# Performance work log

Measured on AMD Instinct MI355X. Metric: run time of the kernel, lower is better.

## Reference

```python
import jax, jax.numpy as jnp
import numpy as np

HEADS = 16
DIM_HEAD = 64
SCALE = DIM_HEAD ** -0.5


def setup_inputs() -> dict:
    key = jax.random.key(0)
    k1, k2, k3, k4 = jax.random.split(key, 4)
    dim = 1024
    inner = HEADS * DIM_HEAD  # 1024
    b, n = 4, 2048
    x = jax.random.normal(k1, (b, n, dim), dtype=jnp.float32)
    # weights stored as [in, out] (equivalent math to torch Linear)
    w_qkv = jax.random.normal(k2, (dim, inner * 3), dtype=jnp.float32) * (dim ** -0.5)
    w_out = jax.random.normal(k3, (inner, dim), dtype=jnp.float32) * (inner ** -0.5)
    b_out = jax.random.normal(k4, (dim,), dtype=jnp.float32) * 0.01
    return {"x": x, "w_qkv": w_qkv, "w_out": w_out, "b_out": b_out}


def reference(x, w_qkv, w_out, b_out):
    b, n, dim = x.shape
    qkv = x @ w_qkv                                   # [b, n, 3*inner]
    q, k, v = jnp.split(qkv, 3, axis=-1)
    def to_heads(t):
        return t.reshape(b, n, HEADS, DIM_HEAD).transpose(0, 2, 1, 3)  # b h n d
    q, k, v = to_heads(q) * SCALE, to_heads(k), to_heads(v)
    dots = jnp.einsum('bhid,bhjd->bhij', q, k)        # [b, h, n, n]
    mask_value = -jnp.finfo(dots.dtype).max
    causal_mask = jnp.triu(jnp.ones((n, n), dtype=bool), k=1)
    dots = jnp.where(causal_mask, mask_value, dots)
    attn = jax.nn.softmax(dots, axis=-1)
    out = jnp.einsum('bhij,bhjd->bhid', attn, v)      # [b, h, n, d]
    out = out.transpose(0, 2, 1, 3).reshape(b, n, HEADS * DIM_HEAD)
    return out @ w_out + b_out
```

## Files before the change

### kernel.cpp

```cpp
#include <hip/hip_runtime.h>
#include <hip/hip_bf16.h>
#include <stdint.h>

typedef __attribute__((ext_vector_type(8))) short bf16x8;
typedef __attribute__((ext_vector_type(4))) float f32x4;
typedef __attribute__((ext_vector_type(4))) unsigned int uint32x4;

#define TOKENS 8192
#define DMODEL 1024
#define NQKV   3072
#define NSEQ   2048
#define NHEAD  16
#define DHEAD  64

__device__ __forceinline__ ushort f32_bf16(float f) {
    uint32_t u = __builtin_bit_cast(uint32_t, f);
    u = (u + 0x7fffu + ((u >> 16) & 1u)) >> 16;
    return (ushort)u;
}

__device__ __forceinline__ unsigned int cvt_pk_bf16(float lo, float hi) {
    unsigned int r;
    asm("v_cvt_pk_bf16_f32 %0, %1, %2" : "=v"(r) : "v"(lo), "v"(hi));
    return r;
}
__device__ __forceinline__ void permlane32_swap(unsigned int& a, unsigned int& b) {
    asm("v_permlane32_swap_b32 %0, %1" : "+v"(a), "+v"(b));
}
__device__ __forceinline__ void permlane16_swap(unsigned int& a, unsigned int& b) {
    asm("v_permlane16_swap_b32 %0, %1" : "+v"(a), "+v"(b));
}
__device__ __forceinline__ unsigned opaque_copy(unsigned x) {
    unsigned y;
    asm("v_mov_b32 %0, %1" : "=v"(y) : "v"(x));
    return y;
}

__device__ __forceinline__ float red_max_g(float x) {
    unsigned a = __builtin_bit_cast(unsigned, x);
    unsigned b = opaque_copy(a);
    permlane16_swap(a, b);
    float r = fmaxf(__builtin_bit_cast(float, a), __builtin_bit_cast(float, b));
    unsigned c = __builtin_bit_cast(unsigned, r);
    unsigned d = opaque_copy(c);
    permlane32_swap(c, d);
    return fmaxf(__builtin_bit_cast(float, c), __builtin_bit_cast(float, d));
}
__device__ __forceinline__ float red_sum_g(float x) {
    unsigned a = __builtin_bit_cast(unsigned, x);
    unsigned b = opaque_copy(a);
    permlane16_swap(a, b);
    float r = __builtin_bit_cast(float, a) + __builtin_bit_cast(float, b);
    unsigned c = __builtin_bit_cast(unsigned, r);
    unsigned d = opaque_copy(c);
    permlane32_swap(c, d);
    return __builtin_bit_cast(float, c) + __builtin_bit_cast(float, d);
}

__device__ __forceinline__ void gload16(const void* g, void* l) {
    __builtin_amdgcn_global_load_lds(
        (const __attribute__((address_space(1))) void*)g,
        (__attribute__((address_space(3))) void*)l, 16, 0, 0);
}

__device__ __forceinline__ void barf() {
    asm volatile("" ::: "memory");
    __builtin_amdgcn_s_barrier();
    asm volatile("" ::: "memory");
}

__global__ void cvt_x_kernel(const float* __restrict__ x, ushort* __restrict__ xb) {
    int i = blockIdx.x * 256 + threadIdx.x;
    float4 v = reinterpret_cast<const float4*>(x)[i];
    ushort4 o;
    o.x = f32_bf16(v.x); o.y = f32_bf16(v.y);
    o.z = f32_bf16(v.z); o.w = f32_bf16(v.w);
    reinterpret_cast<ushort4*>(xb)[i] = o;
}

__global__ __launch_bounds__(256) void cvt_wt_kernel(
    const float* __restrict__ w, ushort* __restrict__ wt, int N)
{
    __shared__ float tile[64][65];
    const int tid = threadIdx.x;
    const int r  = tid >> 4;
    const int c4 = (tid & 15) * 4;
    const int n0 = blockIdx.x * 64;
    const int k0 = blockIdx.y * 64;
    #pragma unroll
    for (int i = 0; i < 4; ++i) {
        const float4 v = *reinterpret_cast<const float4*>(&w[(size_t)(k0 + r + i * 16) * N + n0 + c4]);
        tile[r + i * 16][c4 + 0] = v.x;
        tile[r + i * 16][c4 + 1] = v.y;
        tile[r + i * 16][c4 + 2] = v.z;
        tile[r + i * 16][c4 + 3] = v.w;
    }
    __syncthreads();
    #pragma unroll
    for (int i = 0; i < 4; ++i) {
        ushort4 o;
        o.x = f32_bf16(tile[c4 + 0][r + i * 16]);
        o.y = f32_bf16(tile[c4 + 1][r + i * 16]);
        o.z = f32_bf16(tile[c4 + 2][r + i * 16]);
        o.w = f32_bf16(tile[c4 + 3][r + i * 16]);
        *reinterpret_cast<ushort4*>(&wt[(size_t)(n0 + r + i * 16) * 1024 + k0 + c4]) = o;
    }
}

template<int MODE>
__global__ __launch_bounds__(256) void gemm_bt(
    const ushort* __restrict__ A, const ushort* __restrict__ Bt,
    ushort* __restrict__ Qb, ushort* __restrict__ Kb, ushort* __restrict__ Vtb,
    float* __restrict__ Out, const float* __restrict__ bias)
{
    constexpr int K = 1024;
    __shared__ __align__(16) ushort As[2][128 * 32];
    __shared__ __align__(16) ushort Bs[2][128 * 32];

    const int lane = threadIdx.x & 63;
    const int w    = threadIdx.x >> 6;
    const int l16  = lane & 15;
    const int g    = lane >> 4;
    const int row0 = blockIdx.y * 128;
    const int col0 = blockIdx.x * 128;
    const int wr   = (w >> 1) * 64;
    const int wc   = (w & 1) * 64;

    const int srow  = w * 16 + (lane >> 2);
    const int sswz8 = ((lane & 3) ^ ((lane >> 3) & 3)) * 8;
    const ushort* Ag = A  + (size_t)(row0 + srow) * K + sswz8;
    const ushort* Bg = Bt + (size_t)(col0 + srow) * K + sswz8;
    const int woff = w * (16 * 32);

    const int cq8 = (g ^ ((l16 >> 1) & 3)) * 8;

    f32x4 acc[4][4] = {};

#define GSTAGE(BUF, KK) do {                                             \
        gload16(Ag + (KK),          &As[BUF][woff]);                     \
        gload16(Ag + 64 * K + (KK), &As[BUF][woff + 64 * 32]);           \
        gload16(Bg + (KK),          &Bs[BUF][woff]);                     \
        gload16(Bg + 64 * K + (KK), &Bs[BUF][woff + 64 * 32]);           \
    } while (0)

#define GCOMPUTE(BUF) do {                                               \
        bf16x8 a[4], b[4];                                               \
        _Pragma("unroll")                                                \
        for (int m = 0; m < 4; ++m)                                      \
            a[m] = *reinterpret_cast<const bf16x8*>(                     \
                &As[BUF][(wr + m * 16 + l16) * 32 + cq8]);               \
        _Pragma("unroll")                                                \
        for (int n = 0; n < 4; ++n)                                      \
            b[n] = *reinterpret_cast<const bf16x8*>(                     \
                &Bs[BUF][(wc + n * 16 + l16) * 32 + cq8]);               \
        _Pragma("unroll")                                                \
        for (int m = 0; m < 4; ++m)                                      \
            _Pragma("unroll")                                            \
            for (int n = 0; n < 4; ++n)                                  \
                acc[m][n] = __builtin_amdgcn_mfma_f32_16x16x32_bf16(     \
                    a[m], b[n], acc[m][n], 0, 0, 0);                     \
    } while (0)

    GSTAGE(0, 0);
    GSTAGE(1, 32);
    for (int kk = 0; kk + 128 <= K; kk += 64) {
        asm volatile("s_waitcnt vmcnt(4)" ::: "memory");
        barf();
        GCOMPUTE(0);
        barf();
        GSTAGE(0, kk + 64);
        asm volatile("s_waitcnt vmcnt(4)" ::: "memory");
        barf();
        GCOMPUTE(1);
        barf();
        GSTAGE(1, kk + 96);
    }
    asm volatile("s_waitcnt vmcnt(4)" ::: "memory");
    barf();
    GCOMPUTE(0);
    asm volatile("s_waitcnt vmcnt(0)" ::: "memory");
    barf();
    GCOMPUTE(1);
#undef GSTAGE
#undef GCOMPUTE

    if (MODE == 0) {
        const int part = col0 >> 10;
        const float QSC = 0.18033688011112042f;
        #pragma unroll
        for (int m = 0; m < 4; ++m) {
            const int trow = row0 + wr + m * 16 + 4 * g;
            #pragma unroll
            for (int n = 0; n < 4; ++n) {
                const int c  = col0 + wc + n * 16 + l16;
                const int cc = c & 1023;
                const int h  = cc >> 6, d = cc & 63;
                #pragma unroll
                for (int jj = 0; jj < 4; ++jj) {
                    const int t  = trow + jj;
                    const int bb = t >> 11, nn = t & 2047;
                    const float v = acc[m][n][jj];
                    const size_t bhid = (size_t)(bb * NHEAD + h);
                    if (part == 0)
                        Qb[(bhid * NSEQ + nn) * DHEAD + d] = f32_bf16(v * QSC);
                    else if (part == 1)
                        Kb[(bhid * NSEQ + nn) * DHEAD + d] = f32_bf16(v);
                    else
                        Vtb[bhid * (NSEQ * DHEAD) + (size_t)(nn >> 5) * (DHEAD * 32)
                            + d * 32 + (nn & 31)] = f32_bf16(v);
                }
            }
        }
    } else {
        #pragma unroll
        for (int m = 0; m < 4; ++m) {
            const int trow = row0 + wr + m * 16 + 4 * g;
            #pragma unroll
            for (int n = 0; n < 4; ++n) {
                const int c = col0 + wc + n * 16 + l16;
                const float bv = bias[c];
                #pragma unroll
                for (int jj = 0; jj < 4; ++jj)
                    Out[(size_t)(trow + jj) * DMODEL + c] = acc[m][n][jj] + bv;
            }
        }
    }
}

__device__ __forceinline__ void attn_qk(
    int kt, int qr0s, int l16, int g,
    const bf16x8 (&kk)[4][2],
    const bf16x8 qf0, const bf16x8 qf1,
    f32x4 (&oacc)[4], float& mrun, float& lsum,
    bf16x8& pf0, bf16x8& pf1)
{
    const f32x4 zero = {};
    f32x4 s[4];
    __builtin_amdgcn_s_setprio(1);
    #pragma unroll
    for (int t = 0; t < 4; ++t) {
        s[t] = __builtin_amdgcn_mfma_f32_16x16x32_bf16(kk[t][0], qf0, zero, 0, 0, 0);
        s[t] = __builtin_amdgcn_mfma_f32_16x16x32_bf16(kk[t][1], qf1, s[t], 0, 0, 0);
    }
    __builtin_amdgcn_s_setprio(0);
    if (kt + 63 > qr0s) {
        const int kb = kt + 4 * g - (qr0s + l16);
        #pragma unroll
        for (int t = 0; t < 4; ++t)
            #pragma unroll
            for (int jj = 0; jj < 4; ++jj)
                if (kb + 16 * t + jj > 0) s[t][jj] = -1e30f;
    }
    const float m0 = fmaxf(fmaxf(s[0][0], s[0][1]), s[0][2]);
    const float m1 = fmaxf(fmaxf(s[0][3], s[1][0]), s[1][1]);
    const float m2 = fmaxf(fmaxf(s[1][2], s[1][3]), s[2][0]);
    const float m3 = fmaxf(fmaxf(s[2][1], s[2][2]), s[2][3]);
    const float m4 = fmaxf(fmaxf(s[3][0], s[3][1]), s[3][2]);
    const float m5 = fmaxf(fmaxf(m0, m1), m2);
    const float m6 = fmaxf(fmaxf(m3, m4), s[3][3]);
    const float mxl = fmaxf(m5, m6);
    if (__any(mxl > mrun + 8.0f)) {
        const float mx = red_max_g(mxl);
        const float mn = fmaxf(mrun, mx);
        const float sc = __builtin_amdgcn_exp2f(mrun - mn);
        mrun = mn;
        lsum *= sc;
        float scj[4];
        #pragma unroll
        for (int jj = 0; jj < 4; ++jj) scj[jj] = __shfl(sc, 4 * g + jj);
        #pragma unroll
        for (int dt = 0; dt < 4; ++dt)
            #pragma unroll
            for (int jj = 0; jj < 4; ++jj) oacc[dt][jj] *= scj[jj];
    }
    float ps = 0.f;
    unsigned int pw[4][2];
    #pragma unroll
    for (int t = 0; t < 4; ++t) {
        const float p0 = __builtin_amdgcn_exp2f(s[t][0] - mrun);
        const float p1 = __builtin_amdgcn_exp2f(s[t][1] - mrun);
        const float p2 = __builtin_amdgcn_exp2f(s[t][2] - mrun);
        const float p3 = __builtin_amdgcn_exp2f(s[t][3] - mrun);
        ps += (p0 + p1) + (p2 + p3);
        pw[t][0] = cvt_pk_bf16(p0, p1);
        pw[t][1] = cvt_pk_bf16(p2, p3);
    }
    lsum += ps;
    unsigned int a0 = pw[0][0], a1 = pw[0][1], b0 = pw[1][0], b1 = pw[1][1];
    permlane32_swap(a0, b0); permlane32_swap(a1, b1);
    permlane16_swap(a0, b0); permlane16_swap(a1, b1);
    pf0 = __builtin_bit_cast(bf16x8, (uint32x4){a0, a1, b0, b1});
    unsigned int c0 = pw[2][0], c1 = pw[2][1], d0 = pw[3][0], d1 = pw[3][1];
    permlane32_swap(c0, d0); permlane32_swap(c1, d1);
    permlane16_swap(c0, d0); permlane16_swap(c1, d1);
    pf1 = __builtin_bit_cast(bf16x8, (uint32x4){c0, c1, d0, d1});
}

__global__ __launch_bounds__(256) void attn_kernel(
    const ushort* __restrict__ Qb, const ushort* __restrict__ Kb,
    const ushort* __restrict__ Vt, ushort* __restrict__ Ob)
{
    __shared__ __align__(16) ushort Klds[2][4096];
    __shared__ __align__(16) ushort Vlds[2][4096];

    const int lane = threadIdx.x & 63;
    const int w    = threadIdx.x >> 6;
    const int l16  = lane & 15;
    const int g    = lane >> 4;

    const int bid = blockIdx.x;
    const int xcd = bid & 7, ii = bid >> 3;
    const int bh  = xcd * 8 + (ii >> 4);
    const int jlo = ii & 15;
    const int jhi = 31 - jlo;

    const int qr0_lo = jlo * 64 + w * 16;
    const int qr0_hi = jhi * 64 + w * 16;
    const int nt = jhi + 1;

    const ushort* QpL = Qb + ((size_t)bh * NSEQ + qr0_lo + l16) * DHEAD + 8 * g;
    const ushort* QpH = Qb + ((size_t)bh * NSEQ + qr0_hi + l16) * DHEAD + 8 * g;
    const bf16x8 qfL0 = *reinterpret_cast<const bf16x8*>(QpL);
    const bf16x8 qfL1 = *reinterpret_cast<const bf16x8*>(QpL + 32);
    const bf16x8 qfH0 = *reinterpret_cast<const bf16x8*>(QpH);
    const bf16x8 qfH1 = *reinterpret_cast<const bf16x8*>(QpH + 32);

    const ushort* Kg = Kb + (size_t)bh * (NSEQ * DHEAD);
    const ushort* Vg = Vt + (size_t)bh * (NSEQ * DHEAD);

    const int q0    = w * 2;
    const int srow  = lane >> 2;
    const int sswz8 = ((lane & 3) ^ ((lane >> 3) & 3)) * 8;
    const int cq8   = (g ^ ((l16 >> 1) & 3)) * 8;

    f32x4 oaccL[4] = {}, oaccH[4] = {};
    float mrunL = -1e30f, lsumL = 0.f, mrunH = -1e30f, lsumH = 0.f;

    #pragma unroll
    for (int i = 0; i < 2; ++i) {
        const int q = q0 + i;
        gload16(Kg + (size_t)((q & 3) * 16 + srow) * 64 + (q >> 2) * 32 + sswz8,
                &Klds[0][q * 512]);
        gload16(Vg + (size_t)(q >> 2) * 2048 + ((q & 3) * 16 + srow) * 32 + sswz8,
                &Vlds[0][q * 512]);
    }
    __syncthreads();

    for (int t = 0; t < nt; ++t) {
        const int cur = t & 1;
        if (t + 1 < nt) {
            const int kt1 = (t + 1) * 64;
            #pragma unroll
            for (int i = 0; i < 2; ++i) {
                const int q = q0 + i;
                gload16(Kg + (size_t)(kt1 + (q & 3) * 16 + srow) * 64 + (q >> 2) * 32 + sswz8,
                        &Klds[cur ^ 1][q * 512]);
                gload16(Vg + (size_t)kt1 * 64 + (q >> 2) * 2048 + ((q & 3) * 16 + srow) * 32 + sswz8,
                        &Vlds[cur ^ 1][q * 512]);
            }
        }
        const int kt = t * 64;
        bf16x8 kk[4][2];
        #pragma unroll
        for (int tt = 0; tt < 4; ++tt) {
            #pragma unroll
            for (int h = 0; h < 2; ++h)
                kk[tt][h] = *reinterpret_cast<const bf16x8*>(
                    &Klds[cur][h * 2048 + (16 * tt + l16) * 32 + cq8]);
        }
        bf16x8 pfH0, pfH1, pfL0, pfL1;
        attn_qk(kt, qr0_hi, l16, g, kk, qfH0, qfH1, oaccH, mrunH, lsumH, pfH0, pfH1);
        const bool doLo = (t <= jlo);
        if (doLo)
            attn_qk(kt, qr0_lo, l16, g, kk, qfL0, qfL1, oaccL, mrunL, lsumL, pfL0, pfL1);
        __builtin_amdgcn_s_setprio(1);
        #pragma unroll
        for (int dt = 0; dt < 4; ++dt) {
            const bf16x8 v0 = *reinterpret_cast<const bf16x8*>(
                &Vlds[cur][(dt * 16 + l16) * 32 + cq8]);
            const bf16x8 v1 = *reinterpret_cast<const bf16x8*>(
                &Vlds[cur][2048 + (dt * 16 + l16) * 32 + cq8]);
            oaccH[dt] = __builtin_amdgcn_mfma_f32_16x16x32_bf16(pfH0, v0, oaccH[dt], 0, 0, 0);
            oaccH[dt] = __builtin_amdgcn_mfma_f32_16x16x32_bf16(pfH1, v1, oaccH[dt], 0, 0, 0);
            if (doLo) {
                oaccL[dt] = __builtin_amdgcn_mfma_f32_16x16x32_bf16(pfL0, v0, oaccL[dt], 0, 0, 0);
                oaccL[dt] = __builtin_amdgcn_mfma_f32_16x16x32_bf16(pfL1, v1, oaccL[dt], 0, 0, 0);
            }
        }
        __builtin_amdgcn_s_setprio(0);
        __syncthreads();
    }

    const int bb = bh >> 4, h = bh & 15;
    {
        const float inv = 1.0f / red_sum_g(lsumH);
        float invj[4];
        #pragma unroll
        for (int jj = 0; jj < 4; ++jj) invj[jj] = __shfl(inv, 4 * g + jj);
        #pragma unroll
        for (int jj = 0; jj < 4; ++jj) {
            const size_t t = (size_t)bb * NSEQ + qr0_hi + 4 * g + jj;
            #pragma unroll
            for (int dt = 0; dt < 4; ++dt)
                Ob[t * DMODEL + h * DHEAD + dt * 16 + l16] = f32_bf16(oaccH[dt][jj] * invj[jj]);
        }
    }
    {
        const float inv = 1.0f / red_sum_g(lsumL);
        float invj[4];
        #pragma unroll
        for (int jj = 0; jj < 4; ++jj) invj[jj] = __shfl(inv, 4 * g + jj);
        #pragma unroll
        for (int jj = 0; jj < 4; ++jj) {
            const size_t t = (size_t)bb * NSEQ + qr0_lo + 4 * g + jj;
            #pragma unroll
            for (int dt = 0; dt < 4; ++dt)
                Ob[t * DMODEL + h * DHEAD + dt * 16 + l16] = f32_bf16(oaccL[dt][jj] * invj[jj]);
        }
    }
}

extern "C" void kernel_launch(void* const* d_in, const int* in_sizes, int n_in,
                              void* d_out, int out_size, void* d_ws, size_t ws_size,
                              hipStream_t stream)
{
    const float* x     = (const float*)d_in[0];
    const float* w_qkv = (const float*)d_in[1];
    const float* w_out = (const float*)d_in[2];
    const float* b_out = (const float*)d_in[3];
    float* out = (float*)d_out;

    char* ws = (char*)d_ws;
    ushort* x_bf   = (ushort*)(ws);
    ushort* wqkv_t = (ushort*)(ws + 16777216);
    ushort* wout_t = (ushort*)(ws + 23068672);
    ushort* q_bf   = (ushort*)(ws + 25165824);
    ushort* k_bf   = (ushort*)(ws + 41943040);
    ushort* vt_bf  = (ushort*)(ws + 58720256);
    ushort* attn_bf = x_bf;

    cvt_x_kernel<<<dim3(TOKENS * DMODEL / 4 / 256), dim3(256), 0, stream>>>(x, x_bf);
    cvt_wt_kernel<<<dim3(NQKV / 64, 1024 / 64), dim3(256), 0, stream>>>(w_qkv, wqkv_t, NQKV);
    cvt_wt_kernel<<<dim3(1024 / 64, 1024 / 64), dim3(256), 0, stream>>>(w_out, wout_t, 1024);

    gemm_bt<0><<<dim3(NQKV / 128, TOKENS / 128), dim3(256), 0, stream>>>(
        x_bf, wqkv_t, q_bf, k_bf, vt_bf, nullptr, nullptr);

    attn_kernel<<<dim3(1024), dim3(256), 0, stream>>>(q_bf, k_bf, vt_bf, attn_bf);

    gemm_bt<1><<<dim3(DMODEL / 128, TOKENS / 128), dim3(256), 0, stream>>>(
        attn_bf, wout_t, nullptr, nullptr, nullptr, out, b_out);
}
```

Baseline: 208.9 us.

## Replace QKV GEMM with 256x256-tile, 512-thread kernel with swizzled block order

Adds a dedicated QKV projection GEMM that uses 256x256 output tiles, 8 waves per block, 64-wide K stages double-buffered in LDS with an XOR swizzle, and a phase-interleaved schedule that overlaps global loads with MFMA work. It also remaps block indices so that neighbouring blocks share input panels. The larger tile is meant to raise arithmetic intensity and cut redundant global and L2 traffic compared with the 128x128 template. The cost is more registers (128 accumulator floats per lane) and about 128KB of LDS per block, which limits occupancy to one block per CU. The output projection GEMM keeps the old kernel, now split out as its own non-template function.

```diff
diff --git a/kernel.cpp b/kernel.cpp
--- a/kernel.cpp
+++ b/kernel.cpp
@@ -107,10 +107,136 @@
     }
 }
 
-template<int MODE>
-__global__ __launch_bounds__(256) void gemm_bt(
+__global__ __launch_bounds__(512) void gemm256_qkv(
     const ushort* __restrict__ A, const ushort* __restrict__ Bt,
-    ushort* __restrict__ Qb, ushort* __restrict__ Kb, ushort* __restrict__ Vtb,
+    ushort* __restrict__ Qb, ushort* __restrict__ Kb, ushort* __restrict__ Vtb)
+{
+    constexpr int K = 1024;
+    __shared__ __align__(16) ushort Alds[2][2][128 * 64];
+    __shared__ __align__(16) ushort Blds[2][2][128 * 64];
+
+    const int tid  = threadIdx.x;
+    const int lane = tid & 63;
+    const int w    = tid >> 6;
+    const int l16  = lane & 15;
+    const int g    = lane >> 4;
+
+    const int gidx = (blockIdx.x & 7) * 48 + (blockIdx.x >> 3);
+    const int row0 = (gidx & 31) * 256;
+    const int col0 = (gidx >> 5) * 256;
+
+    const int wm   = w >> 2;
+    const int wn   = w & 3;
+    const int wrow = wm * 128;
+    const int wcol = wn * 64;
+
+    const int c0   = w * 2;
+    const int srow = lane >> 3;
+    const int sq   = ((lane & 7) ^ srow) * 8;
+    const ushort* Abase = A  + (size_t)(row0 + srow) * K + sq;
+    const ushort* Bbase = Bt + (size_t)(col0 + srow) * K + sq;
+
+    f32x4 acc[8][4] = {};
+    bf16x8 bfr[4][2];
+
+#define STAGE_A2(T) do { const size_t _k = (size_t)(T) * 64;                  \
+        gload16(Abase + _k + (size_t)(c0 * 8) * K,         &Alds[(T)&1][0][c0 * 512]);       \
+        gload16(Abase + _k + (size_t)((c0 + 1) * 8) * K,   &Alds[(T)&1][0][(c0 + 1) * 512]); \
+        gload16(Abase + _k + (size_t)(128 + c0 * 8) * K,   &Alds[(T)&1][1][c0 * 512]);       \
+        gload16(Abase + _k + (size_t)(128 + (c0 + 1) * 8) * K, &Alds[(T)&1][1][(c0 + 1) * 512]); \
+    } while (0)
+#define STAGE_B2(T) do { const size_t _k = (size_t)(T) * 64;                  \
+        gload16(Bbase + _k + (size_t)(c0 * 8) * K,         &Blds[(T)&1][0][c0 * 512]);       \
+        gload16(Bbase + _k + (size_t)((c0 + 1) * 8) * K,   &Blds[(T)&1][0][(c0 + 1) * 512]); \
+        gload16(Bbase + _k + (size_t)(128 + c0 * 8) * K,   &Blds[(T)&1][1][c0 * 512]);       \
+        gload16(Bbase + _k + (size_t)(128 + (c0 + 1) * 8) * K, &Blds[(T)&1][1][(c0 + 1) * 512]); \
+    } while (0)
+
+#define RD_A(D, M, KS) (*reinterpret_cast<const bf16x8*>(                     \
+    &Alds[D][wm][((M) * 16 + l16) * 64 + ((((KS) * 4 + g) ^ (l16 & 7)) * 8)]))
+#define RD_B(D, N, KS) (*reinterpret_cast<const bf16x8*>(                     \
+    &Blds[D][wn >> 1][((wn & 1) * 64 + (N) * 16 + l16) * 64 + ((((KS) * 4 + g) ^ (l16 & 7)) * 8)]))
+
+#define PHASE(D, MB, LOADB, STMT, VMSTMT) do {                                \
+        bf16x8 af00 = RD_A(D, MB, 0),     af01 = RD_A(D, MB, 1);              \
+        bf16x8 af10 = RD_A(D, (MB) + 1, 0), af11 = RD_A(D, (MB) + 1, 1);      \
+        if (LOADB) {                                                          \
+            _Pragma("unroll")                                                 \
+            for (int n = 0; n < 4; ++n) {                                     \
+                bfr[n][0] = RD_B(D, n, 0);                                    \
+                bfr[n][1] = RD_B(D, n, 1);                                    \
+            }                                                                 \
+        }                                                                     \
+        STMT;                                                                 \
+        barf();                                                               \
+        __builtin_amdgcn_s_setprio(1);                                        \
+        _Pragma("unroll")                                                     \
+        for (int n = 0; n < 4; ++n) {                                         \
+            acc[MB][n]       = __builtin_amdgcn_mfma_f32_16x16x32_bf16(af00, bfr[n][0], acc[MB][n], 0, 0, 0);       \
+            acc[MB][n]       = __builtin_amdgcn_mfma_f32_16x16x32_bf16(af01, bfr[n][1], acc[MB][n], 0, 0, 0);       \
+            acc[(MB) + 1][n] = __builtin_amdgcn_mfma_f32_16x16x32_bf16(af10, bfr[n][0], acc[(MB) + 1][n], 0, 0, 0); \
+            acc[(MB) + 1][n] = __builtin_amdgcn_mfma_f32_16x16x32_bf16(af11, bfr[n][1], acc[(MB) + 1][n], 0, 0, 0); \
+        }                                                                     \
+        __builtin_amdgcn_s_setprio(0);                                        \
+        VMSTMT;                                                               \
+        barf();                                                               \
+    } while (0)
+
+    STAGE_B2(0); STAGE_A2(0); STAGE_B2(1);
+    asm volatile("s_waitcnt vmcnt(4)" ::: "memory");
+    barf();
+
+    for (int i = 0; i < 8; ++i) {
+        const int ta = 2 * i, tb = 2 * i + 1;
+        const bool more = (i < 7);
+        PHASE(0, 0, true,  { STAGE_A2(tb); }, );
+        PHASE(0, 2, false, { if (more) STAGE_B2(ta + 2); }, );
+        PHASE(0, 4, false, , );
+        PHASE(0, 6, false, ,
+              { if (more) asm volatile("s_waitcnt vmcnt(4)" ::: "memory");
+                else      asm volatile("s_waitcnt vmcnt(0)" ::: "memory"); });
+        PHASE(1, 0, true,  { if (more) STAGE_A2(ta + 2); }, );
+        PHASE(1, 2, false, { if (more) STAGE_B2(tb + 2); }, );
+        PHASE(1, 4, false, , );
+        PHASE(1, 6, false, ,
+              { if (more) asm volatile("s_waitcnt vmcnt(4)" ::: "memory"); });
+    }
+#undef PHASE
+#undef RD_A
+#undef RD_B
+#undef STAGE_A2
+#undef STAGE_B2
+
+    const float QSC = 0.18033688011112042f;
+    const int part = col0 >> 10;
+    #pragma unroll
+    for (int m = 0; m < 8; ++m) {
+        const int trow = row0 + wrow + m * 16 + 4 * g;
+        #pragma unroll
+        for (int n = 0; n < 4; ++n) {
+            const int c  = col0 + wcol + n * 16 + l16;
+            const int cc = c & 1023;
+            const int h  = cc >> 6, d = cc & 63;
+            #pragma unroll
+            for (int jj = 0; jj < 4; ++jj) {
+                const int t  = trow + jj;
+                const int bb = t >> 11, nn = t & 2047;
+                const float v = acc[m][n][jj];
+                const size_t bhid = (size_t)(bb * NHEAD + h);
+                if (part == 0)
+                    Qb[(bhid * NSEQ + nn) * DHEAD + d] = f32_bf16(v * QSC);
+                else if (part == 1)
+                    Kb[(bhid * NSEQ + nn) * DHEAD + d] = f32_bf16(v);
+                else
+                    Vtb[bhid * (NSEQ * DHEAD) + (size_t)(nn >> 5) * (DHEAD * 32)
+                        + d * 32 + (nn & 31)] = f32_bf16(v);
+            }
+        }
+    }
+}
+
+__global__ __launch_bounds__(256) void gemm_out(
+    const ushort* __restrict__ A, const ushort* __restrict__ Bt,
     float* __restrict__ Out, const float* __restrict__ bias)
 {
     constexpr int K = 1024;
@@ -131,7 +257,6 @@
     const ushort* Ag = A  + (size_t)(row0 + srow) * K + sswz8;
     const ushort* Bg = Bt + (size_t)(col0 + srow) * K + sswz8;
     const int woff = w * (16 * 32);
-
     const int cq8 = (g ^ ((l16 >> 1) & 3)) * 8;
 
     f32x4 acc[4][4] = {};
@@ -142,7 +267,6 @@
         gload16(Bg + (KK),          &Bs[BUF][woff]);                     \
         gload16(Bg + 64 * K + (KK), &Bs[BUF][woff + 64 * 32]);           \
     } while (0)
-
 #define GCOMPUTE(BUF) do {                                               \
         bf16x8 a[4], b[4];                                               \
         _Pragma("unroll")                                                \
@@ -184,45 +308,16 @@
 #undef GSTAGE
 #undef GCOMPUTE
 
-    if (MODE == 0) {
-        const int part = col0 >> 10;
-        const float QSC = 0.18033688011112042f;
-        #pragma unroll
-        for (int m = 0; m < 4; ++m) {
-            const int trow = row0 + wr + m * 16 + 4 * g;
-            #pragma unroll
-            for (int n = 0; n < 4; ++n) {
-                const int c  = col0 + wc + n * 16 + l16;
-                const int cc = c & 1023;
-                const int h  = cc >> 6, d = cc & 63;
-                #pragma unroll
-                for (int jj = 0; jj < 4; ++jj) {
-                    const int t  = trow + jj;
-                    const int bb = t >> 11, nn = t & 2047;
-                    const float v = acc[m][n][jj];
-                    const size_t bhid = (size_t)(bb * NHEAD + h);
-                    if (part == 0)
-                        Qb[(bhid * NSEQ + nn) * DHEAD + d] = f32_bf16(v * QSC);
-                    else if (part == 1)
-                        Kb[(bhid * NSEQ + nn) * DHEAD + d] = f32_bf16(v);
-                    else
-                        Vtb[bhid * (NSEQ * DHEAD) + (size_t)(nn >> 5) * (DHEAD * 32)
-                            + d * 32 + (nn & 31)] = f32_bf16(v);
-                }
-            }
-        }
-    } else {
-        #pragma unroll
-        for (int m = 0; m < 4; ++m) {
-            const int trow = row0 + wr + m * 16 + 4 * g;
-            #pragma unroll
-            for (int n = 0; n < 4; ++n) {
-                const int c = col0 + wc + n * 16 + l16;
-                const float bv = bias[c];
-                #pragma unroll
-                for (int jj = 0; jj < 4; ++jj)
-                    Out[(size_t)(trow + jj) * DMODEL + c] = acc[m][n][jj] + bv;
-            }
+    #pragma unroll
+    for (int m = 0; m < 4; ++m) {
+        const int trow = row0 + wr + m * 16 + 4 * g;
+        #pragma unroll
+        for (int n = 0; n < 4; ++n) {
+            const int c = col0 + wc + n * 16 + l16;
+            const float bv = bias[c];
+            #pragma unroll
+            for (int jj = 0; jj < 4; ++jj)
+                Out[(size_t)(trow + jj) * DMODEL + c] = acc[m][n][jj] + bv;
         }
     }
 }
@@ -443,11 +538,11 @@
     cvt_wt_kernel<<<dim3(NQKV / 64, 1024 / 64), dim3(256), 0, stream>>>(w_qkv, wqkv_t, NQKV);
     cvt_wt_kernel<<<dim3(1024 / 64, 1024 / 64), dim3(256), 0, stream>>>(w_out, wout_t, 1024);
 
-    gemm_bt<0><<<dim3(NQKV / 128, TOKENS / 128), dim3(256), 0, stream>>>(
-        x_bf, wqkv_t, q_bf, k_bf, vt_bf, nullptr, nullptr);
+    gemm256_qkv<<<dim3((TOKENS / 256) * (NQKV / 256)), dim3(512), 0, stream>>>(
+        x_bf, wqkv_t, q_bf, k_bf, vt_bf);
 
     attn_kernel<<<dim3(1024), dim3(256), 0, stream>>>(q_bf, k_bf, vt_bf, attn_bf);
 
-    gemm_bt<1><<<dim3(DMODEL / 128, TOKENS / 128), dim3(256), 0, stream>>>(
-        attn_bf, wout_t, nullptr, nullptr, nullptr, out, b_out);
-}
+    gemm_out<<<dim3(DMODEL / 128, TOKENS / 128), dim3(256), 0, stream>>>(
+        attn_bf, wout_t, out, b_out);
+}
```

Measured after the change: 239.3 us. +14.5%, slower.
